# Kernel tuning notes

Hardware: AMD Instinct MI355X
Metric: run time of the kernel (lower is better)

## Reference

```python
import jax, jax.numpy as jnp
import numpy as np
from jax import lax

B_BLK = 16   # block size B
N_Z = 64     # latent dim


def setup_inputs() -> dict:
    key = jax.random.key(0)
    ks = jax.random.split(key, 6)
    in_ch, out_ch = 256, 256
    L = (out_ch // B_BLK) * (in_ch // B_BLK)  # 256 latent codes
    x = jax.random.normal(ks[0], (32, in_ch, 64, 64), dtype=jnp.float32)
    z = jax.random.normal(ks[1], (L, N_Z), dtype=jnp.float32)
    W1 = jax.random.normal(ks[2], (B_BLK, N_Z, N_Z), dtype=jnp.float32) * 0.1
    B1 = jax.random.normal(ks[3], (B_BLK, N_Z), dtype=jnp.float32) * 0.1
    W2 = jax.random.normal(ks[4], (B_BLK, B_BLK * 9, N_Z), dtype=jnp.float32) * 0.1
    B2 = jax.random.normal(ks[5], (B_BLK, B_BLK * 9), dtype=jnp.float32) * 0.1
    return {"x": x, "z": z, "W1": W1, "B1": B1, "W2": W2, "B2": B2}


def _aggregate_weight(z, W1, B1, W2, B2, out_ch, in_ch):
    # hypertype='separate', batched over all L = (out_ch//B)*(in_ch//B) blocks.
    # per block: a = W1 @ z + B1 -> (B, N_z); K = W2 @ a[...,None] + B2 -> (B, B*9)
    a = jnp.einsum('bdn,ln->lbd', W1, z) + B1            # (L, B, N_z)
    K = jnp.einsum('bkd,lbd->lbk', W2, a) + B2           # (L, B, B*9)
    ob, ib = out_ch // B_BLK, in_ch // B_BLK
    K = K.reshape(ob, ib, B_BLK, B_BLK, 3, 3)            # (o_blk, i_blk, b1, b2, 3, 3)
    # torch: K.reshape(B,B,3,3).permute(1,0,2,3) => weight_block[p,q] = K[q,p]
    # then cat over i_blk on dim 1 (in), over o_blk on dim 0 (out)
    w = K.transpose(0, 3, 1, 2, 4, 5)                    # (o_blk, b2, i_blk, b1, 3, 3)
    return w.reshape(out_ch, in_ch, 3, 3)


def reference(x, z, W1, B1, W2, B2):
    out_ch, in_ch = 256, 256
    weight = _aggregate_weight(z, W1, B1, W2, B2, out_ch, in_ch)
    # F.conv2d(x, weight, bias=None, stride=1, padding=kernel_size//2=1)
    return lax.conv_general_dilated(
        x, weight,
        window_strides=(1, 1),
        padding=[(1, 1), (1, 1)],
        dimension_numbers=('NCHW', 'OIHW', 'NCHW'))
```

## Files before the change

kernel.cpp:

```cpp
#include <hip/hip_runtime.h>

typedef unsigned short u16;
typedef unsigned int u32;
typedef __attribute__((ext_vector_type(8))) short short8;
typedef __attribute__((ext_vector_type(4))) float f32x4;

__device__ __forceinline__ u16 f2bf(float f) {
    u32 u = __float_as_uint(f);
    return (u16)((u + 0x7FFFu + ((u >> 16) & 1u)) >> 16);
}

__device__ __forceinline__ void gld16(const u16* g, u16* l) {
    __builtin_amdgcn_global_load_lds(
        (const __attribute__((address_space(1))) unsigned int*)(unsigned long long)(const void*)g,
        (__attribute__((address_space(3))) unsigned int*)(unsigned long long)(void*)l,
        16, 0, 0);
}

__global__ __launch_bounds__(256) void nchw2nhwc_pad(const float* __restrict__ x,
                                                     u16* __restrict__ xp) {
    __shared__ float tile[64][66];
    const int tid = threadIdx.x;
    const int b   = blockIdx.x;
    const int n   = b >> 8;
    const int icb = (b >> 6) & 3;
    const int row = b & 63;
    const int ic0 = icb * 64;

    const int q = tid & 15, r0 = tid >> 4;
    const float* src = x + (size_t)(n * 256 + ic0) * 4096 + row * 64 + q * 4;
#pragma unroll
    for (int rr = 0; rr < 4; ++rr) {
        const int r = r0 + rr * 16;
        const float4 v = *(const float4*)(src + (size_t)r * 4096);
        float2* t0 = (float2*)&tile[r][q * 4];
        t0[0] = make_float2(v.x, v.y);
        t0[1] = make_float2(v.z, v.w);
    }
    __syncthreads();

    const int c = tid & 7, ph = tid >> 3;
    u16* dst = xp + ((size_t)n * 4356 + (size_t)(row + 1) * 66 + 1) * 256 + ic0 + c * 8;
#pragma unroll
    for (int pp = 0; pp < 2; ++pp) {
        const int p = ph + pp * 32;
        u32 w0[4];
#pragma unroll
        for (int k = 0; k < 4; ++k) {
            const float f0 = tile[c * 8 + 2 * k][p];
            const float f1 = tile[c * 8 + 2 * k + 1][p];
            w0[k] = ((u32)f2bf(f1) << 16) | f2bf(f0);
        }
        uint4 v4; v4.x = w0[0]; v4.y = w0[1]; v4.z = w0[2]; v4.w = w0[3];
        *(uint4*)(dst + (size_t)p * 256) = v4;
    }

    u16* hrow = xp + ((size_t)n * 4356 + (size_t)(row + 1) * 66) * 256 + ic0;
    if (tid < 64) {
        const int wp = (tid >> 5) ? 65 : 0;
        *(u32*)(hrow + (size_t)wp * 256 + (tid & 31) * 2) = 0u;
    }
    if (row == 0) {
        u16* tb = xp + (size_t)n * 4356 * 256 + ic0;
        for (int i = tid; i < 2112; i += 256)
            *(u32*)(tb + (size_t)(i >> 5) * 256 + (i & 31) * 2) = 0u;
    }
    if (row == 63) {
        u16* bb = xp + ((size_t)n * 4356 + 65 * 66) * 256 + ic0;
        for (int i = tid; i < 2112; i += 256)
            *(u32*)(bb + (size_t)(i >> 5) * 256 + (i & 31) * 2) = 0u;
    }
}

__global__ __launch_bounds__(256) void wgen(const float* __restrict__ z,
                                            const float* __restrict__ W1,
                                            const float* __restrict__ B1,
                                            const float* __restrict__ W2,
                                            const float* __restrict__ B2,
                                            u16* __restrict__ wb) {
    __shared__ float zl[64];
    __shared__ float aL[1024];
    const int l = blockIdx.x;
    const int tid = threadIdx.x;
    if (tid < 64) zl[tid] = z[l * 64 + tid];
    __syncthreads();
#pragma unroll
    for (int i = 0; i < 4; ++i) {
        int idx = i * 256 + tid;
        const float* wrow = W1 + (size_t)idx * 64;
        float s = B1[idx];
        for (int nn = 0; nn < 64; ++nn) s += wrow[nn] * zl[nn];
        aL[idx] = s;
    }
    __syncthreads();
    const int b1 = tid >> 4, b2 = tid & 15;
    const int ob = l >> 4, ib = l & 15;
    const int ic = ib * 16 + b1;
    const int oc = ob * 16 + b2;
    const size_t wbase = (size_t)oc * 2304 + ic;
    const float* arow = aL + b1 * 64;
#pragma unroll
    for (int tap = 0; tap < 9; ++tap) {
        int kk = b2 * 9 + tap;
        const float* w2row = W2 + (size_t)(b1 * 144 + kk) * 64;
        float s = B2[b1 * 144 + kk];
        for (int d = 0; d < 64; ++d) s += w2row[d] * arow[d];
        wb[wbase + (size_t)tap * 256] = f2bf(s);
    }
}

__global__ __launch_bounds__(256) void conv_mfma(const u16* __restrict__ xp,
                                                 const u16* __restrict__ wb,
                                                 float* __restrict__ out) {
    __shared__ __align__(16) u16 As[2][128 * 32];
    __shared__ __align__(16) u16 Bs[2][128 * 32];

    const int tid = threadIdx.x;
    const int b0  = blockIdx.x;
    const int bid = (b0 & 7) * 256 + (b0 >> 3);
    const int mt = bid & 1;
    const int nt = bid >> 1;
    const int n = nt >> 5;
    const int pimg = (nt & 31) << 7;
    const int oc0 = mt << 7;

    const int lane = tid & 63;
    const int wave = tid >> 6;
    const int wm = (wave >> 1) & 1, wn = wave & 1;
    const int lr = lane & 15, lq = lane >> 4;
    const int sw = (lq ^ (lr & 3)) * 8;

    const int ls = lane >> 2;
    const int swst = ((lane & 3) ^ (ls & 3)) * 8;
    const int rr0 = wave * 32 + ls;
    const int rr1 = rr0 + 16;
    const u16* wbA0 = wb + (size_t)(oc0 + rr0) * 2304 + swst;
    const u16* wbA1 = wb + (size_t)(oc0 + rr1) * 2304 + swst;
    const int p0 = pimg + rr0, p1 = pimg + rr1;
    const int pb0 = ((p0 >> 6) + 1) * 66 + (p0 & 63) + 1;
    const int pb1 = ((p1 >> 6) + 1) * 66 + (p1 & 63) + 1;
    const u16* xpN = xp + (size_t)n * 4356 * 256 + swst;

    auto stage = [&](int bi, int kt) {
        const int tap = kt >> 3, icb = kt & 7;
        const int t3 = tap / 3;
        const int dh = t3 - 1, dw = tap - t3 * 3 - 1;
        const int ko = tap * 256 + icb * 32;
        const int bo = (dh * 66 + dw) * 256 + icb * 32;
        u16* ab = &As[bi][wave * 1024];
        u16* bb = &Bs[bi][wave * 1024];
        gld16(wbA0 + ko, ab);
        gld16(wbA1 + ko, ab + 512);
        gld16(xpN + (pb0 * 256 + bo), bb);
        gld16(xpN + (pb1 * 256 + bo), bb + 512);
    };

    f32x4 acc[4][4];
    const f32x4 z4 = {0.f, 0.f, 0.f, 0.f};
#pragma unroll
    for (int i = 0; i < 4; ++i)
#pragma unroll
        for (int j = 0; j < 4; ++j) acc[i][j] = z4;

    stage(0, 0);
#pragma unroll 2
    for (int kt = 0; kt < 72; ++kt) {
        const int cur = kt & 1;
        __syncthreads();
        if (kt < 71) stage(cur ^ 1, kt + 1);

        const u16* Ab = &As[cur][0];
        const u16* Bb = &Bs[cur][0];
        short8 af[4], bf[4];
#pragma unroll
        for (int i = 0; i < 4; ++i) {
            af[i] = *(const short8*)(Ab + (wm * 64 + i * 16 + lr) * 32 + sw);
            bf[i] = *(const short8*)(Bb + (wn * 64 + i * 16 + lr) * 32 + sw);
        }
#pragma unroll
        for (int i = 0; i < 4; ++i)
#pragma unroll
            for (int j = 0; j < 4; ++j)
                acc[i][j] = __builtin_amdgcn_mfma_f32_16x16x32_bf16(
                    af[i], bf[j], acc[i][j], 0, 0, 0);
    }

    const size_t outn = (size_t)n * 256 * 4096;
#pragma unroll
    for (int i = 0; i < 4; ++i) {
        const int ocb = oc0 + wm * 64 + i * 16 + lq * 4;
#pragma unroll
        for (int j = 0; j < 4; ++j) {
            const int po = pimg + wn * 64 + j * 16 + lr;
            float* op = out + outn + (size_t)ocb * 4096 + po;
#pragma unroll
            for (int r = 0; r < 4; ++r) op[(size_t)r * 4096] = acc[i][j][r];
        }
    }
}

extern "C" void kernel_launch(void* const* d_in, const int* in_sizes, int n_in,
                              void* d_out, int out_size, void* d_ws, size_t ws_size,
                              hipStream_t stream) {
    const float* x  = (const float*)d_in[0];
    const float* z  = (const float*)d_in[1];
    const float* W1 = (const float*)d_in[2];
    const float* B1 = (const float*)d_in[3];
    const float* W2 = (const float*)d_in[4];
    const float* B2 = (const float*)d_in[5];
    float* out = (float*)d_out;

    u16* xp = (u16*)d_ws;
    u16* wb = xp + (size_t)32 * 4356 * 256;
    const size_t need = ((size_t)32 * 4356 * 256 + (size_t)256 * 2304) * 2;
    if (ws_size < need) return;

    nchw2nhwc_pad<<<dim3(8192), dim3(256), 0, stream>>>(x, xp);
    wgen<<<dim3(256), dim3(256), 0, stream>>>(z, W1, B1, W2, B2, wb);
    conv_mfma<<<dim3(2048), dim3(256), 0, stream>>>(xp, wb, out);
}
```

Before: 448.8 us.

## Restructure weight-generation kernel to stage W1/W2 slices in shared memory

Result: faster. 426.8 us (-4.9%).

```diff
diff --git a/kernel.cpp b/kernel.cpp
--- a/kernel.cpp
+++ b/kernel.cpp
@@ -78,34 +78,79 @@
                                             const float* __restrict__ W2,
                                             const float* __restrict__ B2,
                                             u16* __restrict__ wb) {
-    __shared__ float zl[64];
-    __shared__ float aL[1024];
-    const int l = blockIdx.x;
+    __shared__ float zl[64][65];
+    __shared__ float w1s[4096];
+    __shared__ float aS[64][65];
+    __shared__ float w2s[9216];
+
     const int tid = threadIdx.x;
-    if (tid < 64) zl[tid] = z[l * 64 + tid];
+    const int b   = blockIdx.x >> 2;
+    const int lc  = blockIdx.x & 3;
+    const int l   = tid & 63;
+    const int g   = tid >> 6;
+
+    const float* zg  = z  + (size_t)lc * 4096;
+    const float* w1g = W1 + (size_t)b * 4096;
+    const float* w2g = W2 + (size_t)b * 9216;
+#pragma unroll
+    for (int k = 0; k < 4; ++k) {
+        const int i4 = tid + k * 256;
+        const float4 v = *(const float4*)(zg + (size_t)i4 * 4);
+        const int lr = i4 >> 4, nr = (i4 * 4) & 63;
+        zl[lr][nr] = v.x; zl[lr][nr + 1] = v.y; zl[lr][nr + 2] = v.z; zl[lr][nr + 3] = v.w;
+        *(float4*)(w1s + (size_t)i4 * 4) = *(const float4*)(w1g + (size_t)i4 * 4);
+    }
+#pragma unroll
+    for (int k = 0; k < 9; ++k) {
+        const int i4 = tid + k * 256;
+        *(float4*)(w2s + (size_t)i4 * 4) = *(const float4*)(w2g + (size_t)i4 * 4);
+    }
     __syncthreads();
-#pragma unroll
-    for (int i = 0; i < 4; ++i) {
-        int idx = i * 256 + tid;
-        const float* wrow = W1 + (size_t)idx * 64;
-        float s = B1[idx];
-        for (int nn = 0; nn < 64; ++nn) s += wrow[nn] * zl[nn];
-        aL[idx] = s;
+
+    {
+        float acc[16];
+#pragma unroll
+        for (int j = 0; j < 16; ++j) acc[j] = B1[b * 64 + g * 16 + j];
+#pragma unroll
+        for (int nb = 0; nb < 16; ++nb) {
+            float zv0 = zl[l][nb * 4 + 0];
+            float zv1 = zl[l][nb * 4 + 1];
+            float zv2 = zl[l][nb * 4 + 2];
+            float zv3 = zl[l][nb * 4 + 3];
+#pragma unroll
+            for (int j = 0; j < 16; ++j) {
+                const float4 w = *(const float4*)(w1s + (g * 16 + j) * 64 + nb * 4);
+                acc[j] += w.x * zv0 + w.y * zv1 + w.z * zv2 + w.w * zv3;
+            }
+        }
+#pragma unroll
+        for (int j = 0; j < 16; ++j) aS[l][g * 16 + j] = acc[j];
     }
     __syncthreads();
-    const int b1 = tid >> 4, b2 = tid & 15;
-    const int ob = l >> 4, ib = l & 15;
-    const int ic = ib * 16 + b1;
-    const int oc = ob * 16 + b2;
-    const size_t wbase = (size_t)oc * 2304 + ic;
-    const float* arow = aL + b1 * 64;
-#pragma unroll
-    for (int tap = 0; tap < 9; ++tap) {
-        int kk = b2 * 9 + tap;
-        const float* w2row = W2 + (size_t)(b1 * 144 + kk) * 64;
-        float s = B2[b1 * 144 + kk];
-        for (int d = 0; d < 64; ++d) s += w2row[d] * arow[d];
-        wb[wbase + (size_t)tap * 256] = f2bf(s);
+
+    float acc2[36];
+#pragma unroll
+    for (int t = 0; t < 36; ++t) acc2[t] = B2[b * 144 + g * 36 + t];
+#pragma unroll
+    for (int db = 0; db < 16; ++db) {
+        float av0 = aS[l][db * 4 + 0];
+        float av1 = aS[l][db * 4 + 1];
+        float av2 = aS[l][db * 4 + 2];
+        float av3 = aS[l][db * 4 + 3];
+#pragma unroll
+        for (int t = 0; t < 36; ++t) {
+            const float4 w = *(const float4*)(w2s + (g * 36 + t) * 64 + db * 4);
+            acc2[t] += w.x * av0 + w.y * av1 + w.z * av2 + w.w * av3;
+        }
+    }
+
+    const int lg = lc * 64 + l;
+    const int ob = lg >> 4, ib = lg & 15;
+#pragma unroll
+    for (int t = 0; t < 36; ++t) {
+        const int b2 = 4 * g + t / 9;
+        const int tap = t % 9;
+        wb[(size_t)(ob * 16 + b2) * 2304 + tap * 256 + ib * 16 + b] = f2bf(acc2[t]);
     }
 }
 
@@ -216,6 +261,6 @@
     if (ws_size < need) return;
 
     nchw2nhwc_pad<<<dim3(8192), dim3(256), 0, stream>>>(x, xp);
-    wgen<<<dim3(256), dim3(256), 0, stream>>>(z, W1, B1, W2, B2, wb);
+    wgen<<<dim3(64), dim3(256), 0, stream>>>(z, W1, B1, W2, B2, wb);
     conv_mfma<<<dim3(2048), dim3(256), 0, stream>>>(xp, wb, out);
 }
```
